# Optimization experiments

Measured on AMD Instinct MI355X. Metric: run time of the kernel, lower is better.

## Reference

```python
import jax, jax.numpy as jnp
import numpy as np

D = 128      # state_dim
ED = 20      # edge_dim (RBF basis size)
R = 3        # num message/update rounds
G = 3        # gated equivariant blocks
CUT = 5.0    # cutoff
N = 10000    # nodes
E = 160000   # edges
B = 500      # molecules
HRO = 64     # readout hidden


def setup_inputs() -> dict:
    key = jax.random.key(0)
    ks = jax.random.split(key, 40)
    sc = 0.05

    def nrm(k, shape):
        return jax.random.normal(k, shape, dtype=jnp.float32) * sc

    inp = {
        "h": jax.random.normal(ks[0], (N, 5), dtype=jnp.float32),
        "pos": jax.random.normal(ks[1], (N, 3), dtype=jnp.float32),
        "edge_index": jax.random.randint(ks[2], (2, E), 0, N),
        "batch": jnp.sort(jax.random.randint(ks[3], (N,), 0, B)),
        # node embedding Linear(5, D)
        "emb_w": nrm(ks[4], (5, D)), "emb_b": nrm(ks[5], (D,)),
        # per-round message params (stacked over rounds)
        "msg_phi_w1": nrm(ks[6], (R, D, D)), "msg_phi_b1": nrm(ks[7], (R, D)),
        "msg_phi_w2": nrm(ks[8], (R, D, 3 * D)), "msg_phi_b2": nrm(ks[9], (R, 3 * D)),
        "msg_filt_w": nrm(ks[10], (R, ED, 3 * D)), "msg_filt_b": nrm(ks[11], (R, 3 * D)),
        # per-round update params
        "upd_U": nrm(ks[12], (R, D, D)), "upd_V": nrm(ks[13], (R, D, D)),
        "upd_w1": nrm(ks[14], (R, 2 * D, D)), "upd_b1": nrm(ks[15], (R, D)),
        "upd_w2": nrm(ks[16], (R, D, 3 * D)), "upd_b2": nrm(ks[17], (R, 3 * D)),
        # gated equivariant blocks
        "geb_wv1": nrm(ks[18], (G, D, D)), "geb_wv2": nrm(ks[19], (G, D, D)),
        "geb_w1": nrm(ks[20], (G, 2 * D, D)), "geb_b1": nrm(ks[21], (G, D)),
        "geb_w2": nrm(ks[22], (G, D, 2 * D)), "geb_b2": nrm(ks[23], (G, 2 * D)),
        # invariant readout MLP
        "ro_w1": nrm(ks[24], (D, HRO)), "ro_b1": nrm(ks[25], (HRO,)),
        "ro_w2": nrm(ks[26], (HRO, 1)), "ro_b2": nrm(ks[27], (1,)),
    }
    return inp


def _safe_norm(x, axis):
    return jnp.sqrt(jnp.sum(x * x, axis=axis) + 1e-8)


def reference(h, pos, edge_index, batch,
              emb_w, emb_b,
              msg_phi_w1, msg_phi_b1, msg_phi_w2, msg_phi_b2,
              msg_filt_w, msg_filt_b,
              upd_U, upd_V, upd_w1, upd_b1, upd_w2, upd_b2,
              geb_wv1, geb_wv2, geb_w1, geb_b1, geb_w2, geb_b2,
              ro_w1, ro_b1, ro_w2, ro_b2):
    n_nodes = h.shape[0]
    row, col = edge_index[0], edge_index[1]
    # edge vectors: r_ij = pos[col] - pos[row]
    r_ij = pos[col] - pos[row]                                   # [E,3]
    d = jnp.clip(jnp.linalg.norm(r_ij, axis=1, keepdims=True), 1e-6, None)  # [E,1]
    unit = r_ij / d                                              # [E,3]
    # sinc radial basis + cosine cutoff
    freqs = jnp.arange(1, ED + 1, dtype=h.dtype)
    rbf = jnp.sin(freqs * jnp.pi * d / CUT) / d                  # [E,ED]
    fcut = 0.5 * (jnp.cos(jnp.pi * d / CUT) + 1.0) * (d < CUT)   # [E,1]

    s = h @ emb_w + emb_b                                        # [N,D]
    v = jnp.zeros((n_nodes, D, 3), dtype=h.dtype)                # [N,D,3]

    for r in range(R):
        # --- PaiNNMessage ---
        phi = jax.nn.silu(s @ msg_phi_w1[r] + msg_phi_b1[r]) @ msg_phi_w2[r] + msg_phi_b2[r]  # [N,3D]
        filt = (rbf @ msg_filt_w[r] + msg_filt_b[r]) * fcut      # [E,3D]
        x = phi[col] * filt                                      # gather + modulate  [E,3D]
        xs, xvv, xvw = jnp.split(x, 3, axis=-1)                  # each [E,D]
        ds = jax.ops.segment_sum(xs, row, num_segments=n_nodes)  # [N,D]
        dv_e = xvv[:, :, None] * v[col] + xvw[:, :, None] * unit[:, None, :]  # [E,D,3]
        dv = jax.ops.segment_sum(dv_e, row, num_segments=n_nodes)             # [N,D,3]
        s = s + ds
        v = v + dv
        # --- PaiNNUpdate ---
        Uv = jnp.einsum('ndc,de->nec', v, upd_U[r])              # [N,D,3]
        Vv = jnp.einsum('ndc,de->nec', v, upd_V[r])              # [N,D,3]
        Vn = _safe_norm(Vv, axis=-1)                             # [N,D]
        a = jax.nn.silu(jnp.concatenate([s, Vn], axis=-1) @ upd_w1[r] + upd_b1[r]) @ upd_w2[r] + upd_b2[r]
        a_ss, a_sv, a_vv = jnp.split(a, 3, axis=-1)
        s = s + a_ss + a_sv * jnp.sum(Uv * Vv, axis=-1)
        v = v + a_vv[:, :, None] * Uv

    # --- GatedEquivariantBlocks ---
    for g in range(G):
        v1 = jnp.einsum('ndc,de->nec', v, geb_wv1[g])
        v2 = jnp.einsum('ndc,de->nec', v, geb_wv2[g])
        n2 = _safe_norm(v2, axis=-1)                             # [N,D]
        a = jax.nn.silu(jnp.concatenate([s, n2], axis=-1) @ geb_w1[g] + geb_b1[g]) @ geb_w2[g] + geb_b2[g]
        s_new, gate = jnp.split(a, 2, axis=-1)
        s = s_new
        v = gate[:, :, None] * v1

    # --- InvariantReadout + molwise scatter ---
    out = jax.nn.silu(s @ ro_w1 + ro_b1) @ ro_w2 + ro_b2         # [N,1]
    molwise = jax.ops.segment_sum(out, batch, num_segments=B)    # [B,1]
    return molwise.squeeze(-1)
```

## Files before the change

### kernel.cpp

```cpp
#include <hip/hip_runtime.h>

typedef __attribute__((ext_vector_type(4))) float f32x4;
typedef __attribute__((ext_vector_type(8))) short short8;

#define D 128
#define D3 384
#define SLD 256
#define EDIM 20
#define KPAD 32
#define NR 3
#define NG 3
#define CUTOFF 5.0f
#define NNODES 10000
#define NEDGES 160000
#define NMOL 500
#define HROH 64
#define PI_F 3.14159265358979323846f

#define FBIAS 1
#define FSILU 2
#define FBF16O 4

static __device__ __forceinline__ float silu_f(float x) {
    return x / (1.0f + expf(-x));
}

static __device__ __forceinline__ ushort f2bf(float x) {
    uint u = __float_as_uint(x);
    uint r = (u + 0x7fffu + ((u >> 16) & 1u)) >> 16;
    return (ushort)r;
}
static __device__ __forceinline__ float bf2f(ushort h) {
    return __uint_as_float((uint)h << 16);
}
static __device__ __forceinline__ uint pack2(float a, float b) {
    return (uint)f2bf(a) | ((uint)f2bf(b) << 16);
}

#define TLR 64
#define TLC 64
#define KC 32
#define APAD 40
#define BPAD 36
#define CPAD 68

struct WSrc { const float* p[12]; };
#define WTOT 880640

__global__ __launch_bounds__(256) void wprep_k(WSrc ws, ushort* __restrict__ dh,
                                               ushort* __restrict__ dl)
{
    const int srcK[12] = {128,128, 20,128,128,256,128,128,128,256,128,128};
    const int dstK[12] = {128,128, 32,128,128,256,128,128,128,256,128,128};
    const int Mm[12]   = {128,384,384,128,128,128,384,128,128,128,256, 64};
    const int nm[12]   = {  3,  3,  3,  3,  3,  3,  3,  3,  3,  3,  3,  1};
    int i = blockIdx.x * 256 + threadIdx.x;
    if (i >= WTOT) return;
    int off = 0, seg = -1, loc = 0;
    #pragma unroll
    for (int s = 0; s < 12; ++s) {
        int sz = nm[s] * Mm[s] * dstK[s];
        if (seg < 0 && i < off + sz) { seg = s; loc = i - off; }
        off += sz;
    }
    int K = dstK[seg], M = Mm[seg], sK = srcK[seg];
    int mat = loc / (M * K);
    int rem = loc - mat * M * K;
    int m = rem / K, k = rem - m * K;
    float v = (k < sK) ? ws.p[seg][(size_t)(mat * sK + k) * M + m] : 0.f;
    ushort h = f2bf(v);
    dh[i] = h;
    dl[i] = f2bf(v - bf2f(h));
}

#define SEG_PHI_W1  0
#define SEG_PHI_W2  49152
#define SEG_FILT_W  196608
#define SEG_UPD_U   233472
#define SEG_UPD_V   282624
#define SEG_UPD_W1  331776
#define SEG_UPD_W2  430080
#define SEG_GEB_WV1 577536
#define SEG_GEB_WV2 626688
#define SEG_GEB_W1  675840
#define SEG_GEB_W2  774144
#define SEG_RO_W1   872448

__global__ __launch_bounds__(256) void gemm_k(
    const float* __restrict__ A, int lda,
    const ushort* __restrict__ Wh, const ushort* __restrict__ Wl, int ldk,
    const float* __restrict__ bias,
    float* __restrict__ C, ushort* __restrict__ Cbf, int ldc,
    int N, int K, int flags)
{
    const int n0 = blockIdx.x * TLR;
    const int m0 = blockIdx.y * TLC;
    __shared__ ushort SM[9728];
    ushort* Ah = SM;
    ushort* Al = SM + 2560;
    ushort* Bh = SM + 5120;
    ushort* Bl = SM + 7424;
    const int tid = threadIdx.x;
    const int arow = tid & 63;
    const int akq = (tid >> 6) * 4;
    const bool aok = (n0 + arow) < N;
    const float* Ar = A + (size_t)(n0 + arow) * lda;
    const int sm = tid & 63;
    const int sq = tid >> 6;
    const ushort* Wph = Wh + (size_t)(m0 + sm) * ldk + sq * 8;
    const ushort* Wpl = Wl + (size_t)(m0 + sm) * ldk + sq * 8;
    const int lane = tid & 63;
    const int wrow = (tid >> 6) * 16;
    const int fr = lane & 15;
    const int kg = lane >> 4;

    f32x4 acc[4];
    #pragma unroll
    for (int t = 0; t < 4; ++t) acc[t] = (f32x4){0.f, 0.f, 0.f, 0.f};

    for (int k0 = 0; k0 < K; k0 += KC) {
        #pragma unroll
        for (int half = 0; half < 2; ++half) {
            int kk = akq + half * 16;
            float4 v = aok ? *(const float4*)(Ar + k0 + kk)
                           : make_float4(0.f, 0.f, 0.f, 0.f);
            ushort h0 = f2bf(v.x), h1 = f2bf(v.y), h2 = f2bf(v.z), h3 = f2bf(v.w);
            ushort l0 = f2bf(v.x - bf2f(h0)), l1 = f2bf(v.y - bf2f(h1));
            ushort l2 = f2bf(v.z - bf2f(h2)), l3 = f2bf(v.w - bf2f(h3));
            uint2 ph, pl;
            ph.x = (uint)h0 | ((uint)h1 << 16); ph.y = (uint)h2 | ((uint)h3 << 16);
            pl.x = (uint)l0 | ((uint)l1 << 16); pl.y = (uint)l2 | ((uint)l3 << 16);
            *(uint2*)(Ah + arow * APAD + kk) = ph;
            *(uint2*)(Al + arow * APAD + kk) = pl;
        }
        {
            uint4 vh = *(const uint4*)(Wph + k0);
            uint4 vl = *(const uint4*)(Wpl + k0);
            ushort* dh = Bh + sm * BPAD + sq * 8;
            ushort* dl = Bl + sm * BPAD + sq * 8;
            *(uint2*)dh       = make_uint2(vh.x, vh.y);
            *(uint2*)(dh + 4) = make_uint2(vh.z, vh.w);
            *(uint2*)dl       = make_uint2(vl.x, vl.y);
            *(uint2*)(dl + 4) = make_uint2(vl.z, vl.w);
        }
        __syncthreads();
        short8 ah = *(const short8*)(Ah + (wrow + fr) * APAD + kg * 8);
        short8 al = *(const short8*)(Al + (wrow + fr) * APAD + kg * 8);
        #pragma unroll
        for (int t = 0; t < 4; ++t) {
            const ushort* bp = Bh + (t * 16 + fr) * BPAD + kg * 8;
            const ushort* bq = Bl + (t * 16 + fr) * BPAD + kg * 8;
            short8 bh, bl;
            ((uint2*)&bh)[0] = *(const uint2*)bp;
            ((uint2*)&bh)[1] = *(const uint2*)(bp + 4);
            ((uint2*)&bl)[0] = *(const uint2*)bq;
            ((uint2*)&bl)[1] = *(const uint2*)(bq + 4);
            acc[t] = __builtin_amdgcn_mfma_f32_16x16x32_bf16(ah, bh, acc[t], 0, 0, 0);
            acc[t] = __builtin_amdgcn_mfma_f32_16x16x32_bf16(al, bh, acc[t], 0, 0, 0);
            acc[t] = __builtin_amdgcn_mfma_f32_16x16x32_bf16(ah, bl, acc[t], 0, 0, 0);
        }
        __syncthreads();
    }

    if (flags & FBF16O) {
        float* Cs = (float*)SM;
        #pragma unroll
        for (int t = 0; t < 4; ++t) {
            #pragma unroll
            for (int r = 0; r < 4; ++r) {
                int row = wrow + kg * 4 + r;
                int n = n0 + row;
                int colm = t * 16 + fr;
                float val = 0.f;
                if (n < N) {
                    val = acc[t][r];
                    if (flags & FBIAS) val += bias[m0 + colm];
                    if (flags & FSILU) val = silu_f(val);
                }
                Cs[row * CPAD + colm] = val;
            }
        }
        __syncthreads();
        #pragma unroll
        for (int it = 0; it < 2; ++it) {
            int chunk = it * 256 + tid;
            int row = chunk >> 3;
            int c8 = (chunk & 7) * 8;
            int n = n0 + row;
            if (n < N) {
                const float* src = Cs + row * CPAD + c8;
                uint4 pk;
                pk.x = pack2(src[0], src[1]);
                pk.y = pack2(src[2], src[3]);
                pk.z = pack2(src[4], src[5]);
                pk.w = pack2(src[6], src[7]);
                *(uint4*)(Cbf + (size_t)n * ldc + m0 + c8) = pk;
            }
        }
    } else {
        #pragma unroll
        for (int t = 0; t < 4; ++t) {
            #pragma unroll
            for (int r = 0; r < 4; ++r) {
                int n = n0 + wrow + kg * 4 + r;
                if (n < N) {
                    int m = m0 + t * 16 + fr;
                    float val = acc[t][r];
                    if (flags & FBIAS) val += bias[m];
                    if (flags & FSILU) val = silu_f(val);
                    C[(size_t)n * ldc + m] = val;
                }
            }
        }
    }
}

__global__ __launch_bounds__(256) void filt_k(
    const float* __restrict__ RBFp,
    const ushort* __restrict__ Wfh,
    const float* __restrict__ bias,
    const float* __restrict__ uf_s,
    const int* __restrict__ col_s,
    const ushort* __restrict__ Pbf,
    ushort* __restrict__ X, int E)
{
    __shared__ ushort Ah[64 * APAD];
    __shared__ ushort Bs[D3 * BPAD];
    __shared__ float  Cs[64 * CPAD];
    __shared__ int    ColS[64];
    const int tid = threadIdx.x;
    const int e0 = blockIdx.x * 64;
    #pragma unroll
    for (int it = 0; it < 2; ++it) {
        int chunk = it * 256 + tid;
        int row = chunk >> 3;
        int kq = (chunk & 7) * 4;
        int e = e0 + row;
        float4 v = (e < E) ? *(const float4*)(RBFp + (size_t)e * KPAD + kq)
                           : make_float4(0.f, 0.f, 0.f, 0.f);
        uint2 ph;
        ph.x = pack2(v.x, v.y);
        ph.y = pack2(v.z, v.w);
        *(uint2*)(Ah + row * APAD + kq) = ph;
    }
    for (int m = tid; m < D3; m += 256) {
        const ushort* s = Wfh + (size_t)m * KPAD;
        ushort* dst = Bs + m * BPAD;
        #pragma unroll
        for (int q = 0; q < 2; ++q) {
            uint4 v = *(const uint4*)(s + q * 16);
            *(uint2*)(dst + q * 16)      = make_uint2(v.x, v.y);
            *(uint2*)(dst + q * 16 + 4)  = make_uint2(v.z, v.w);
            uint4 v2 = *(const uint4*)(s + q * 16 + 8);
            *(uint2*)(dst + q * 16 + 8)  = make_uint2(v2.x, v2.y);
            *(uint2*)(dst + q * 16 + 12) = make_uint2(v2.z, v2.w);
        }
    }
    if (tid < 64) {
        int e = e0 + tid;
        ColS[tid] = (e < E) ? col_s[e] : 0;
    }
    __syncthreads();

    const int lane = tid & 63;
    const int wrow = (tid >> 6) * 16;
    const int fr = lane & 15;
    const int kg = lane >> 4;
    short8 ah = *(const short8*)(Ah + (wrow + fr) * APAD + kg * 8);
    f32x4 acc[24];
    #pragma unroll
    for (int t = 0; t < 24; ++t) {
        const ushort* bp = Bs + (t * 16 + fr) * BPAD + kg * 8;
        short8 bh;
        ((uint2*)&bh)[0] = *(const uint2*)bp;
        ((uint2*)&bh)[1] = *(const uint2*)(bp + 4);
        acc[t] = __builtin_amdgcn_mfma_f32_16x16x32_bf16(
            ah, bh, (f32x4){0.f, 0.f, 0.f, 0.f}, 0, 0, 0);
    }
    float fc[4];
    #pragma unroll
    for (int r = 0; r < 4; ++r) {
        int e = e0 + wrow + kg * 4 + r;
        fc[r] = (e < E) ? uf_s[(size_t)e * 4 + 3] : 0.f;
    }
    for (int ct = 0; ct < 6; ++ct) {
        __syncthreads();
        #pragma unroll
        for (int tt = 0; tt < 4; ++tt) {
            int t = ct * 4 + tt;
            int colm = t * 16 + fr;
            float b = bias[colm];
            #pragma unroll
            for (int r = 0; r < 4; ++r) {
                int row = wrow + kg * 4 + r;
                Cs[row * CPAD + tt * 16 + fr] = (acc[t][r] + b) * fc[r];
            }
        }
        __syncthreads();
        #pragma unroll
        for (int it = 0; it < 2; ++it) {
            int chunk = it * 256 + tid;
            int row = chunk >> 3;
            int c8 = (chunk & 7) * 8;
            int e = e0 + row;
            if (e < E) {
                int mbase = ct * 64 + c8;
                int col = ColS[row];
                uint4 pg = *(const uint4*)(Pbf + (size_t)col * D3 + mbase);
                const float* src = Cs + row * CPAD + c8;
                uint4 pk;
                pk.x = pack2(src[0] * bf2f((ushort)(pg.x & 0xffff)),
                             src[1] * bf2f((ushort)(pg.x >> 16)));
                pk.y = pack2(src[2] * bf2f((ushort)(pg.y & 0xffff)),
                             src[3] * bf2f((ushort)(pg.y >> 16)));
                pk.z = pack2(src[4] * bf2f((ushort)(pg.z & 0xffff)),
                             src[5] * bf2f((ushort)(pg.z >> 16)));
                pk.w = pack2(src[6] * bf2f((ushort)(pg.w & 0xffff)),
                             src[7] * bf2f((ushort)(pg.w >> 16)));
                *(uint4*)(X + (size_t)e * D3 + mbase) = pk;
            }
        }
    }
}

template <bool WITHDOT>
__global__ __launch_bounds__(256) void uvn_k(
    const float* __restrict__ A,
    const ushort* __restrict__ WUh, const ushort* __restrict__ WUl,
    const ushort* __restrict__ WVh, const ushort* __restrict__ WVl,
    float* __restrict__ Uv,
    float* __restrict__ DOT,
    float* __restrict__ SX, int N)
{
    const int n0 = blockIdx.x * 32;
    const int m0 = blockIdx.y * 64;
    __shared__ ushort Ah[3][32 * APAD], Al[3][32 * APAD];
    __shared__ ushort Bh[2][64 * BPAD], Bl[2][64 * BPAD];
    const int tid = threadIdx.x;
    const int arow = tid & 31;
    const int akq = (tid >> 5) * 4;
    const bool aok = (n0 + arow) < N;
    const float* Ar = A + (size_t)(n0 + arow) * D3;
    const int sm = tid & 63;
    const int sq = tid >> 6;
    const int w = tid >> 6;
    const int rt = w & 1;
    const int ch = w >> 1;
    const int lane = tid & 63;
    const int fr = lane & 15;
    const int kg = lane >> 4;

    f32x4 acc[3][2][2];
    #pragma unroll
    for (int c = 0; c < 3; ++c)
        #pragma unroll
        for (int s = 0; s < 2; ++s)
            #pragma unroll
            for (int t = 0; t < 2; ++t) acc[c][s][t] = (f32x4){0.f, 0.f, 0.f, 0.f};

    for (int k0 = 0; k0 < D; k0 += KC) {
        #pragma unroll
        for (int c = 0; c < 3; ++c) {
            float4 v = aok ? *(const float4*)(Ar + c * D + k0 + akq)
                           : make_float4(0.f, 0.f, 0.f, 0.f);
            ushort h0 = f2bf(v.x), h1 = f2bf(v.y), h2 = f2bf(v.z), h3 = f2bf(v.w);
            ushort l0 = f2bf(v.x - bf2f(h0)), l1 = f2bf(v.y - bf2f(h1));
            ushort l2 = f2bf(v.z - bf2f(h2)), l3 = f2bf(v.w - bf2f(h3));
            uint2 ph, pl;
            ph.x = (uint)h0 | ((uint)h1 << 16); ph.y = (uint)h2 | ((uint)h3 << 16);
            pl.x = (uint)l0 | ((uint)l1 << 16); pl.y = (uint)l2 | ((uint)l3 << 16);
            *(uint2*)(&Ah[c][arow * APAD + akq]) = ph;
            *(uint2*)(&Al[c][arow * APAD + akq]) = pl;
        }
        #pragma unroll
        for (int s = 0; s < 2; ++s) {
            const ushort* sh = (s ? WVh : WUh) + (size_t)(m0 + sm) * D + k0 + sq * 8;
            const ushort* sl = (s ? WVl : WUl) + (size_t)(m0 + sm) * D + k0 + sq * 8;
            uint4 vh = *(const uint4*)sh;
            uint4 vl = *(const uint4*)sl;
            ushort* dh = &Bh[s][sm * BPAD + sq * 8];
            ushort* dl = &Bl[s][sm * BPAD + sq * 8];
            *(uint2*)dh       = make_uint2(vh.x, vh.y);
            *(uint2*)(dh + 4) = make_uint2(vh.z, vh.w);
            *(uint2*)dl       = make_uint2(vl.x, vl.y);
            *(uint2*)(dl + 4) = make_uint2(vl.z, vl.w);
        }
        __syncthreads();
        short8 ah[3], al[3];
        #pragma unroll
        for (int c = 0; c < 3; ++c) {
            ah[c] = *(const short8*)(&Ah[c][(rt * 16 + fr) * APAD + kg * 8]);
            al[c] = *(const short8*)(&Al[c][(rt * 16 + fr) * APAD + kg * 8]);
        }
        #pragma unroll
        for (int t = 0; t < 2; ++t) {
            #pragma unroll
            for (int s = 0; s < 2; ++s) {
                const ushort* bp = &Bh[s][(ch * 32 + t * 16 + fr) * BPAD + kg * 8];
                const ushort* bq = &Bl[s][(ch * 32 + t * 16 + fr) * BPAD + kg * 8];
                short8 bh, bl;
                ((uint2*)&bh)[0] = *(const uint2*)bp;
                ((uint2*)&bh)[1] = *(const uint2*)(bp + 4);
                ((uint2*)&bl)[0] = *(const uint2*)bq;
                ((uint2*)&bl)[1] = *(const uint2*)(bq + 4);
                #pragma unroll
                for (int c = 0; c < 3; ++c) {
                    acc[c][s][t] = __builtin_amdgcn_mfma_f32_16x16x32_bf16(ah[c], bh, acc[c][s][t], 0, 0, 0);
                    acc[c][s][t] = __builtin_amdgcn_mfma_f32_16x16x32_bf16(al[c], bh, acc[c][s][t], 0, 0, 0);
                    acc[c][s][t] = __builtin_amdgcn_mfma_f32_16x16x32_bf16(ah[c], bl, acc[c][s][t], 0, 0, 0);
                }
            }
        }
        __syncthreads();
    }
    #pragma unroll
    for (int t = 0; t < 2; ++t) {
        #pragma unroll
        for (int r = 0; r < 4; ++r) {
            int n = n0 + rt * 16 + kg * 4 + r;
            if (n < N) {
                int m = m0 + ch * 32 + t * 16 + fr;
                float ux = acc[0][0][t][r], uy = acc[1][0][t][r], uz = acc[2][0][t][r];
                float vx = acc[0][1][t][r], vy = acc[1][1][t][r], vz = acc[2][1][t][r];
                float* up = Uv + (size_t)n * D3 + m;
                up[0]     = ux;
                up[D]     = uy;
                up[2 * D] = uz;
                SX[(size_t)n * SLD + D + m] =
                    sqrtf(fmaf(vx, vx, fmaf(vy, vy, fmaf(vz, vz, 1e-8f))));
                if (WITHDOT)
                    DOT[(size_t)n * D + m] = fmaf(ux, vx, fmaf(uy, vy, uz * vz));
            }
        }
    }
}

__global__ __launch_bounds__(256) void emb_k(
    const float* __restrict__ h, const float* __restrict__ w,
    const float* __restrict__ b, float* __restrict__ s, int total)
{
    int i = blockIdx.x * 256 + threadIdx.x;
    if (i >= total) return;
    int n = i >> 7, d = i & 127;
    float acc = b[d];
    #pragma unroll
    for (int k = 0; k < 5; ++k) acc = fmaf(h[n * 5 + k], w[k * D + d], acc);
    s[(size_t)n * SLD + d] = acc;
}

__global__ __launch_bounds__(256) void hist_k(const int* __restrict__ ei,
                                              int* __restrict__ cnt, int E)
{
    int e = blockIdx.x * 256 + threadIdx.x;
    if (e < E) atomicAdd(&cnt[ei[e]], 1);
}

__global__ __launch_bounds__(256) void scan_k(const int* __restrict__ cnt,
                                              int* __restrict__ offs, int n)
{
    __shared__ int tmp[256];
    __shared__ int carry;
    if (threadIdx.x == 0) carry = 0;
    __syncthreads();
    for (int base = 0; base < n; base += 256) {
        int i = base + threadIdx.x;
        int v = (i < n) ? cnt[i] : 0;
        tmp[threadIdx.x] = v;
        __syncthreads();
        for (int off = 1; off < 256; off <<= 1) {
            int add = (threadIdx.x >= off) ? tmp[threadIdx.x - off] : 0;
            __syncthreads();
            tmp[threadIdx.x] += add;
            __syncthreads();
        }
        if (i < n) offs[i + 1] = carry + tmp[threadIdx.x];
        __syncthreads();
        if (threadIdx.x == 255) carry += tmp[255];
        __syncthreads();
    }
    if (threadIdx.x == 0) offs[0] = 0;
}

__global__ __launch_bounds__(256) void initnext_k(const int* __restrict__ offs,
                                                  int* __restrict__ next, int n)
{
    int i = blockIdx.x * 256 + threadIdx.x;
    if (i < n) next[i] = offs[i];
}

__global__ __launch_bounds__(256) void edge_pre_k(
    const int* __restrict__ ei, const float* __restrict__ pos,
    int* __restrict__ next, float* __restrict__ rbf_s,
    float* __restrict__ uf_s, int* __restrict__ col_s, int E)
{
    int e = blockIdx.x * 256 + threadIdx.x;
    if (e >= E) return;
    int r = ei[e], c = ei[E + e];
    float dx = pos[c * 3 + 0] - pos[r * 3 + 0];
    float dy = pos[c * 3 + 1] - pos[r * 3 + 1];
    float dz = pos[c * 3 + 2] - pos[r * 3 + 2];
    float dist = sqrtf(dx * dx + dy * dy + dz * dz);
    float d = fmaxf(dist, 1e-6f);
    float inv = 1.0f / d;
    int p = atomicAdd(&next[r], 1);
    col_s[p] = c;
    uf_s[p * 4 + 0] = dx * inv;
    uf_s[p * 4 + 1] = dy * inv;
    uf_s[p * 4 + 2] = dz * inv;
    uf_s[p * 4 + 3] = (d < CUTOFF) ? 0.5f * (cosf(PI_F * d / CUTOFF) + 1.0f) : 0.0f;
    float w = PI_F * d / CUTOFF;
    float* rb = rbf_s + (size_t)p * KPAD;
    #pragma unroll
    for (int k = 1; k <= EDIM; ++k)
        rb[k - 1] = sinf((float)k * w) * inv;
    #pragma unroll
    for (int k = EDIM; k < KPAD; ++k) rb[k] = 0.f;
}

#define MSG_NPB 2
__global__ __launch_bounds__(256) void message_csr_k(
    const int* __restrict__ offs, const int* __restrict__ col_s,
    const ushort* __restrict__ X, const float* __restrict__ uf_s,
    const float* __restrict__ Vold, const ushort* __restrict__ VbfOld,
    float* __restrict__ S, float* __restrict__ Vnew,
    ushort* __restrict__ VbfNew, int N)
{
    const int sub = threadIdx.x >> 7;
    const int d = threadIdx.x & 127;

    auto edge = [&](int j, float& ds, float& dvx, float& dvy, float& dvz) {
        const ushort* xp = X + (size_t)j * D3;
        float xs  = bf2f(xp[d]);
        float xvv = bf2f(xp[D + d]);
        float xvw = bf2f(xp[2 * D + d]);
        int col = col_s[j];
        float4 u4 = *(const float4*)(uf_s + (size_t)j * 4);
        const ushort* vc = VbfOld + (size_t)col * D3;
        ds += xs;
        dvx = fmaf(xvv, bf2f(vc[d]),         fmaf(xvw, u4.x, dvx));
        dvy = fmaf(xvv, bf2f(vc[D + d]),     fmaf(xvw, u4.y, dvy));
        dvz = fmaf(xvv, bf2f(vc[2 * D + d]), fmaf(xvw, u4.z, dvz));
    };

    int n = blockIdx.x * MSG_NPB + sub;
    if (n >= N) return;
    float ds0 = 0.f, dx0 = 0.f, dy0 = 0.f, dz0 = 0.f;
    float ds1 = 0.f, dx1 = 0.f, dy1 = 0.f, dz1 = 0.f;
    const int j0 = offs[n], j1 = offs[n + 1];
    int j = j0;
    for (; j + 2 <= j1; j += 2) {
        edge(j, ds0, dx0, dy0, dz0);
        edge(j + 1, ds1, dx1, dy1, dz1);
    }
    if (j < j1) edge(j, ds0, dx0, dy0, dz0);
    S[(size_t)n * SLD + d] += ds0 + ds1;
    const float* vo = Vold + (size_t)n * D3;
    float* vn = Vnew + (size_t)n * D3;
    ushort* vb = VbfNew + (size_t)n * D3;
    float nx = vo[d] + dx0 + dx1;
    float ny = vo[D + d] + dy0 + dy1;
    float nz = vo[2 * D + d] + dz0 + dz1;
    vn[d] = nx;         vb[d] = f2bf(nx);
    vn[D + d] = ny;     vb[D + d] = f2bf(ny);
    vn[2 * D + d] = nz; vb[2 * D + d] = f2bf(nz);
}

__global__ __launch_bounds__(256) void upd_apply_k(
    const float* __restrict__ U3, const float* __restrict__ DOT,
    const float* __restrict__ P, float* __restrict__ s,
    float* __restrict__ v, ushort* __restrict__ vbf, int total)
{
    int i = blockIdx.x * 256 + threadIdx.x;
    if (i >= total) return;
    int n = i >> 7, d = i & 127;
    const float* u = U3 + (size_t)n * D3;
    float ux = u[d], uy = u[D + d], uz = u[2 * D + d];
    const float* a = P + (size_t)n * D3;
    s[(size_t)n * SLD + d] += a[d] + a[D + d] * DOT[i];
    float avv = a[2 * D + d];
    float* vv = v + (size_t)n * D3;
    ushort* vb = vbf + (size_t)n * D3;
    float nx = fmaf(avv, ux, vv[d]);
    float ny = fmaf(avv, uy, vv[D + d]);
    float nz = fmaf(avv, uz, vv[2 * D + d]);
    vv[d] = nx;         vb[d] = f2bf(nx);
    vv[D + d] = ny;     vb[D + d] = f2bf(ny);
    vv[2 * D + d] = nz; vb[2 * D + d] = f2bf(nz);
}

__global__ __launch_bounds__(256) void geb_apply_k(
    const float* __restrict__ P, const float* __restrict__ U3,
    float* __restrict__ s, float* __restrict__ v, int total)
{
    int i = blockIdx.x * 256 + threadIdx.x;
    if (i >= total) return;
    int n = i >> 7, d = i & 127;
    const float* a = P + (size_t)n * 2 * D;
    s[(size_t)n * SLD + d] = a[d];
    float g = a[D + d];
    const float* u = U3 + (size_t)n * D3;
    float* vv = v + (size_t)n * D3;
    vv[d]         = g * u[d];
    vv[D + d]     = g * u[D + d];
    vv[2 * D + d] = g * u[2 * D + d];
}

__global__ __launch_bounds__(256) void readout_k(
    const float* __restrict__ H2, const float* __restrict__ w2,
    const float* __restrict__ b2, const int* __restrict__ batch,
    float* __restrict__ out, int N)
{
    int n = blockIdx.x * 256 + threadIdx.x;
    if (n >= N) return;
    float acc = b2[0];
    const float* hrow = H2 + (size_t)n * HROH;
    #pragma unroll
    for (int k = 0; k < HROH; ++k) acc = fmaf(hrow[k], w2[k], acc);
    atomicAdd(out + batch[n], acc);
}


static inline void gemm(hipStream_t st, const float* A, int lda,
                        const ushort* Wh, const ushort* Wl, int ldk,
                        const float* bias,
                        float* C, ushort* Cbf, int ldc,
                        int N, int K, int M, int flags)
{
    dim3 g((N + TLR - 1) / TLR, M / TLC, 1);
    hipLaunchKernelGGL(gemm_k, g, dim3(256), 0, st,
                       A, lda, Wh, Wl, ldk, bias, C, Cbf, ldc, N, K, flags);
}

extern "C" void kernel_launch(void* const* d_in, const int* in_sizes, int n_in,
                              void* d_out, int out_size, void* d_ws, size_t ws_size,
                              hipStream_t stream)
{
    const float* h          = (const float*)d_in[0];
    const float* pos        = (const float*)d_in[1];
    const int*   ei         = (const int*)d_in[2];
    const int*   batch      = (const int*)d_in[3];
    const float* emb_w      = (const float*)d_in[4];
    const float* emb_b      = (const float*)d_in[5];
    const float* msg_phi_w1 = (const float*)d_in[6];
    const float* msg_phi_b1 = (const float*)d_in[7];
    const float* msg_phi_w2 = (const float*)d_in[8];
    const float* msg_phi_b2 = (const float*)d_in[9];
    const float* msg_filt_w = (const float*)d_in[10];
    const float* msg_filt_b = (const float*)d_in[11];
    const float* upd_U      = (const float*)d_in[12];
    const float* upd_V      = (const float*)d_in[13];
    const float* upd_w1     = (const float*)d_in[14];
    const float* upd_b1     = (const float*)d_in[15];
    const float* upd_w2     = (const float*)d_in[16];
    const float* upd_b2     = (const float*)d_in[17];
    const float* geb_wv1    = (const float*)d_in[18];
    const float* geb_wv2    = (const float*)d_in[19];
    const float* geb_w1     = (const float*)d_in[20];
    const float* geb_b1     = (const float*)d_in[21];
    const float* geb_w2     = (const float*)d_in[22];
    const float* geb_b2     = (const float*)d_in[23];
    const float* ro_w1      = (const float*)d_in[24];
    const float* ro_b1      = (const float*)d_in[25];
    const float* ro_w2      = (const float*)d_in[26];
    const float* ro_b2      = (const float*)d_in[27];
    float* out = (float*)d_out;

    const int N = NNODES, E = NEDGES;

    char* p = (char*)d_ws;
    auto carve = [&](size_t bytes) {
        char* r = p;
        p += (bytes + 255) & ~(size_t)255;
        return r;
    };
    float*  SX   = (float*)carve((size_t)N * SLD * 4);
    float*  VA   = (float*)carve((size_t)N * D3 * 4);
    float*  VB   = (float*)carve((size_t)N * D3 * 4);
    float*  P_   = (float*)carve((size_t)N * D3 * 4);
    ushort* Pbf  = (ushort*)P_;
    ushort* VBFa = (ushort*)carve((size_t)N * D3 * 2);
    ushort* VBFb = (ushort*)carve((size_t)N * D3 * 2);
    float*  H    = (float*)carve((size_t)N * D * 4);
    float*  H2   = (float*)carve((size_t)N * D * 4);
    float*  RBFp = (float*)carve((size_t)E * KPAD * 4);
    float*  UFs  = (float*)carve((size_t)E * 4 * 4);
    int*    COLs = (int*)carve((size_t)E * 4);
    int*    offs = (int*)carve((size_t)(N + 1) * 4);
    int*    nxt  = (int*)carve((size_t)N * 4);
    ushort* WTH  = (ushort*)carve((size_t)WTOT * 2);
    ushort* WTL  = (ushort*)carve((size_t)WTOT * 2);
    ushort* X    = (ushort*)carve((size_t)E * D3 * 2);

    WSrc wsrc;
    wsrc.p[0] = msg_phi_w1; wsrc.p[1] = msg_phi_w2; wsrc.p[2] = msg_filt_w;
    wsrc.p[3] = upd_U;      wsrc.p[4] = upd_V;      wsrc.p[5] = upd_w1;
    wsrc.p[6] = upd_w2;     wsrc.p[7] = geb_wv1;    wsrc.p[8] = geb_wv2;
    wsrc.p[9] = geb_w1;     wsrc.p[10] = geb_w2;    wsrc.p[11] = ro_w1;
    hipLaunchKernelGGL(wprep_k, dim3((WTOT + 255) / 256), dim3(256), 0, stream,
                       wsrc, WTH, WTL);

    hipMemsetAsync(VA, 0, (size_t)N * D3 * 4, stream);
    hipMemsetAsync(VBFa, 0, (size_t)N * D3 * 2, stream);
    hipLaunchKernelGGL(emb_k, dim3((N * D + 255) / 256), dim3(256), 0, stream,
                       h, emb_w, emb_b, SX, N * D);
    hipMemsetAsync(nxt, 0, (size_t)N * 4, stream);
    hipLaunchKernelGGL(hist_k, dim3((E + 255) / 256), dim3(256), 0, stream, ei, nxt, E);
    hipLaunchKernelGGL(scan_k, dim3(1), dim3(256), 0, stream, nxt, offs, N);
    hipLaunchKernelGGL(initnext_k, dim3((N + 255) / 256), dim3(256), 0, stream,
                       offs, nxt, N);
    hipLaunchKernelGGL(edge_pre_k, dim3((E + 255) / 256), dim3(256), 0, stream,
                       ei, pos, nxt, RBFp, UFs, COLs, E);

    float*  Vc = VA;   ushort* VbfC = VBFa;
    float*  Vs = VB;   ushort* VbfS = VBFb;

    for (int r = 0; r < NR; ++r) {
        gemm(stream, SX, SLD, WTH + SEG_PHI_W1 + (size_t)r * D * D,
             WTL + SEG_PHI_W1 + (size_t)r * D * D, D,
             msg_phi_b1 + (size_t)r * D, H, nullptr, D, N, D, D, FBIAS | FSILU);
        gemm(stream, H, D, WTH + SEG_PHI_W2 + (size_t)r * D * D3,
             WTL + SEG_PHI_W2 + (size_t)r * D * D3, D,
             msg_phi_b2 + (size_t)r * D3, nullptr, Pbf, D3, N, D, D3,
             FBIAS | FBF16O);
        hipLaunchKernelGGL(filt_k, dim3((E + 63) / 64), dim3(256), 0, stream,
                           RBFp, WTH + SEG_FILT_W + (size_t)r * KPAD * D3,
                           msg_filt_b + (size_t)r * D3, UFs, COLs, Pbf, X, E);
        hipLaunchKernelGGL(message_csr_k, dim3((N + MSG_NPB - 1) / MSG_NPB),
                           dim3(256), 0, stream,
                           offs, COLs, X, UFs, Vc, VbfC, SX, Vs, VbfS, N);
        { float* t = Vc; Vc = Vs; Vs = t; }
        { ushort* t = VbfC; VbfC = VbfS; VbfS = t; }
        float* Uv = Vs;
        hipLaunchKernelGGL(HIP_KERNEL_NAME(uvn_k<true>),
                           dim3((N + 31) / 32, 2), dim3(256), 0, stream,
                           Vc, WTH + SEG_UPD_U + (size_t)r * D * D,
                           WTL + SEG_UPD_U + (size_t)r * D * D,
                           WTH + SEG_UPD_V + (size_t)r * D * D,
                           WTL + SEG_UPD_V + (size_t)r * D * D,
                           Uv, H, SX, N);
        gemm(stream, SX, SLD, WTH + SEG_UPD_W1 + (size_t)r * 2 * D * D,
             WTL + SEG_UPD_W1 + (size_t)r * 2 * D * D, 2 * D,
             upd_b1 + (size_t)r * D, H2, nullptr, D, N, 2 * D, D, FBIAS | FSILU);
        gemm(stream, H2, D, WTH + SEG_UPD_W2 + (size_t)r * D * D3,
             WTL + SEG_UPD_W2 + (size_t)r * D * D3, D,
             upd_b2 + (size_t)r * D3, P_, nullptr, D3, N, D, D3, FBIAS);
        hipLaunchKernelGGL(upd_apply_k, dim3((N * D + 255) / 256), dim3(256), 0,
                           stream, Uv, H, P_, SX, Vc, VbfC, N * D);
    }

    for (int g = 0; g < NG; ++g) {
        float* Uv = Vs;
        hipLaunchKernelGGL(HIP_KERNEL_NAME(uvn_k<false>),
                           dim3((N + 31) / 32, 2), dim3(256), 0, stream,
                           Vc, WTH + SEG_GEB_WV1 + (size_t)g * D * D,
                           WTL + SEG_GEB_WV1 + (size_t)g * D * D,
                           WTH + SEG_GEB_WV2 + (size_t)g * D * D,
                           WTL + SEG_GEB_WV2 + (size_t)g * D * D,
                           Uv, nullptr, SX, N);
        gemm(stream, SX, SLD, WTH + SEG_GEB_W1 + (size_t)g * 2 * D * D,
             WTL + SEG_GEB_W1 + (size_t)g * 2 * D * D, 2 * D,
             geb_b1 + (size_t)g * D, H2, nullptr, D, N, 2 * D, D, FBIAS | FSILU);
        gemm(stream, H2, D, WTH + SEG_GEB_W2 + (size_t)g * D * 2 * D,
             WTL + SEG_GEB_W2 + (size_t)g * D * 2 * D, D,
             geb_b2 + (size_t)g * 2 * D, P_, nullptr, 2 * D, N, D, 2 * D, FBIAS);
        hipLaunchKernelGGL(geb_apply_k, dim3((N * D + 255) / 256), dim3(256), 0,
                           stream, P_, Uv, SX, Vc, N * D);
    }

    gemm(stream, SX, SLD, WTH + SEG_RO_W1, WTL + SEG_RO_W1, D,
         ro_b1, H2, nullptr, HROH, N, D, HROH, FBIAS | FSILU);
    hipMemsetAsync(out, 0, (size_t)NMOL * 4, stream);
    hipLaunchKernelGGL(readout_k, dim3((N + 255) / 256), dim3(256), 0, stream,
                       H2, ro_w2, ro_b2, batch, out, N);
}
```

Before: 872.9 us.

## Fuse two-layer MLP GEMM pairs into a single kernel with hidden kept in LDS

Adds a templated mlp_k kernel that computes Linear+SiLU then Linear for a 32-row tile, storing the hidden activation as split bf16 hi/lo in shared memory instead of writing it to global memory. It replaces the phi, update and gated-block GEMM pairs, removing one launch and the H/H2 round-trip per MLP. The cost is fewer blocks (N/32 with one block per row tile), the first-layer weights being reloaded by every block, and a serial loop over output column groups, which may reduce parallelism compared with the 2D-gridded GEMMs.

```diff
diff --git a/kernel.cpp b/kernel.cpp
--- a/kernel.cpp
+++ b/kernel.cpp
@@ -85,6 +85,203 @@
 #define SEG_GEB_W1  675840
 #define SEG_GEB_W2  774144
 #define SEG_RO_W1   872448
+
+template <int K1, int M2, bool OUTBF>
+__global__ __launch_bounds__(256) void mlp_k(
+    const float* __restrict__ A, int lda,
+    const ushort* __restrict__ W1h, const ushort* __restrict__ W1l,
+    const float* __restrict__ b1,
+    const ushort* __restrict__ W2h, const ushort* __restrict__ W2l,
+    const float* __restrict__ b2,
+    float* __restrict__ C, ushort* __restrict__ Cbf, int N)
+{
+    __shared__ char SMB[27648 + 17408];
+    ushort* Ah  = (ushort*)SMB;
+    ushort* Al  = Ah + 1280;
+    ushort* B1h = Ah + 2560;
+    ushort* B1l = B1h + 4608;
+    ushort* Hh  = (ushort*)(SMB + 27648);
+    ushort* Hl  = Hh + 4352;
+
+    const int tid = threadIdx.x;
+    const int n0 = blockIdx.x * 32;
+    const int w = tid >> 6;
+    const int rt = w & 1;
+    const int ch = w >> 1;
+    const int lane = tid & 63;
+    const int fr = lane & 15;
+    const int kg = lane >> 4;
+    const int arow = tid & 31;
+    const int akq = (tid >> 5) * 4;
+    const bool aok = (n0 + arow) < N;
+    const float* Ar = A + (size_t)(n0 + arow) * lda;
+    const int bcol = tid & 127;
+    const int bhalf = tid >> 7;
+
+    f32x4 acc1[4];
+    #pragma unroll
+    for (int t = 0; t < 4; ++t) acc1[t] = (f32x4){0.f, 0.f, 0.f, 0.f};
+
+    for (int k0 = 0; k0 < K1; k0 += KC) {
+        {
+            float4 v = aok ? *(const float4*)(Ar + k0 + akq)
+                           : make_float4(0.f, 0.f, 0.f, 0.f);
+            ushort h0 = f2bf(v.x), h1 = f2bf(v.y), h2 = f2bf(v.z), h3 = f2bf(v.w);
+            ushort l0 = f2bf(v.x - bf2f(h0)), l1 = f2bf(v.y - bf2f(h1));
+            ushort l2 = f2bf(v.z - bf2f(h2)), l3 = f2bf(v.w - bf2f(h3));
+            uint2 ph, pl;
+            ph.x = (uint)h0 | ((uint)h1 << 16); ph.y = (uint)h2 | ((uint)h3 << 16);
+            pl.x = (uint)l0 | ((uint)l1 << 16); pl.y = (uint)l2 | ((uint)l3 << 16);
+            *(uint2*)(Ah + arow * APAD + akq) = ph;
+            *(uint2*)(Al + arow * APAD + akq) = pl;
+        }
+        {
+            const ushort* sh = W1h + (size_t)bcol * K1 + k0 + bhalf * 16;
+            const ushort* sl = W1l + (size_t)bcol * K1 + k0 + bhalf * 16;
+            ushort* dh = B1h + bcol * BPAD + bhalf * 16;
+            ushort* dl = B1l + bcol * BPAD + bhalf * 16;
+            uint4 v0 = *(const uint4*)sh;
+            uint4 v1 = *(const uint4*)(sh + 8);
+            *(uint2*)dh       = make_uint2(v0.x, v0.y);
+            *(uint2*)(dh + 4) = make_uint2(v0.z, v0.w);
+            *(uint2*)(dh + 8) = make_uint2(v1.x, v1.y);
+            *(uint2*)(dh + 12)= make_uint2(v1.z, v1.w);
+            uint4 u0 = *(const uint4*)sl;
+            uint4 u1 = *(const uint4*)(sl + 8);
+            *(uint2*)dl       = make_uint2(u0.x, u0.y);
+            *(uint2*)(dl + 4) = make_uint2(u0.z, u0.w);
+            *(uint2*)(dl + 8) = make_uint2(u1.x, u1.y);
+            *(uint2*)(dl + 12)= make_uint2(u1.z, u1.w);
+        }
+        __syncthreads();
+        short8 ah = *(const short8*)(Ah + (rt * 16 + fr) * APAD + kg * 8);
+        short8 al = *(const short8*)(Al + (rt * 16 + fr) * APAD + kg * 8);
+        #pragma unroll
+        for (int t = 0; t < 4; ++t) {
+            const ushort* bp = B1h + (ch * 64 + t * 16 + fr) * BPAD + kg * 8;
+            const ushort* bq = B1l + (ch * 64 + t * 16 + fr) * BPAD + kg * 8;
+            short8 bh, bl;
+            ((uint2*)&bh)[0] = *(const uint2*)bp;
+            ((uint2*)&bh)[1] = *(const uint2*)(bp + 4);
+            ((uint2*)&bl)[0] = *(const uint2*)bq;
+            ((uint2*)&bl)[1] = *(const uint2*)(bq + 4);
+            acc1[t] = __builtin_amdgcn_mfma_f32_16x16x32_bf16(ah, bh, acc1[t], 0, 0, 0);
+            acc1[t] = __builtin_amdgcn_mfma_f32_16x16x32_bf16(al, bh, acc1[t], 0, 0, 0);
+            acc1[t] = __builtin_amdgcn_mfma_f32_16x16x32_bf16(ah, bl, acc1[t], 0, 0, 0);
+        }
+        __syncthreads();
+    }
+    #pragma unroll
+    for (int t = 0; t < 4; ++t) {
+        int colm = ch * 64 + t * 16 + fr;
+        float b = b1[colm];
+        #pragma unroll
+        for (int r = 0; r < 4; ++r) {
+            int row = rt * 16 + kg * 4 + r;
+            float hv = silu_f(acc1[t][r] + b);
+            ushort hh = f2bf(hv);
+            Hh[row * 136 + colm] = hh;
+            Hl[row * 136 + colm] = f2bf(hv - bf2f(hh));
+        }
+    }
+    __syncthreads();
+
+    ushort* B2h = (ushort*)SMB;
+    ushort* B2l = B2h + 4608;
+    const int NG2 = M2 / 128;
+    for (int g = 0; g < NG2; ++g) {
+        f32x4 acc2[4];
+        #pragma unroll
+        for (int t = 0; t < 4; ++t) acc2[t] = (f32x4){0.f, 0.f, 0.f, 0.f};
+        for (int k0 = 0; k0 < D; k0 += KC) {
+            {
+                const ushort* sh = W2h + (size_t)(g * 128 + bcol) * D + k0 + bhalf * 16;
+                const ushort* sl = W2l + (size_t)(g * 128 + bcol) * D + k0 + bhalf * 16;
+                ushort* dh = B2h + bcol * BPAD + bhalf * 16;
+                ushort* dl = B2l + bcol * BPAD + bhalf * 16;
+                uint4 v0 = *(const uint4*)sh;
+                uint4 v1 = *(const uint4*)(sh + 8);
+                *(uint2*)dh       = make_uint2(v0.x, v0.y);
+                *(uint2*)(dh + 4) = make_uint2(v0.z, v0.w);
+                *(uint2*)(dh + 8) = make_uint2(v1.x, v1.y);
+                *(uint2*)(dh + 12)= make_uint2(v1.z, v1.w);
+                uint4 u0 = *(const uint4*)sl;
+                uint4 u1 = *(const uint4*)(sl + 8);
+                *(uint2*)dl       = make_uint2(u0.x, u0.y);
+                *(uint2*)(dl + 4) = make_uint2(u0.z, u0.w);
+                *(uint2*)(dl + 8) = make_uint2(u1.x, u1.y);
+                *(uint2*)(dl + 12)= make_uint2(u1.z, u1.w);
+            }
+            __syncthreads();
+            short8 ah, al;
+            {
+                const ushort* hp = Hh + (rt * 16 + fr) * 136 + k0 + kg * 8;
+                const ushort* hq = Hl + (rt * 16 + fr) * 136 + k0 + kg * 8;
+                ((uint2*)&ah)[0] = *(const uint2*)hp;
+                ((uint2*)&ah)[1] = *(const uint2*)(hp + 4);
+                ((uint2*)&al)[0] = *(const uint2*)hq;
+                ((uint2*)&al)[1] = *(const uint2*)(hq + 4);
+            }
+            #pragma unroll
+            for (int t = 0; t < 4; ++t) {
+                const ushort* bp = B2h + (ch * 64 + t * 16 + fr) * BPAD + kg * 8;
+                const ushort* bq = B2l + (ch * 64 + t * 16 + fr) * BPAD + kg * 8;
+                short8 bh, bl;
+                ((uint2*)&bh)[0] = *(const uint2*)bp;
+                ((uint2*)&bh)[1] = *(const uint2*)(bp + 4);
+                ((uint2*)&bl)[0] = *(const uint2*)bq;
+                ((uint2*)&bl)[1] = *(const uint2*)(bq + 4);
+                acc2[t] = __builtin_amdgcn_mfma_f32_16x16x32_bf16(ah, bh, acc2[t], 0, 0, 0);
+                acc2[t] = __builtin_amdgcn_mfma_f32_16x16x32_bf16(al, bh, acc2[t], 0, 0, 0);
+                acc2[t] = __builtin_amdgcn_mfma_f32_16x16x32_bf16(ah, bl, acc2[t], 0, 0, 0);
+            }
+            __syncthreads();
+        }
+        if (OUTBF) {
+            float* Cs = (float*)SMB;
+            #pragma unroll
+            for (int t = 0; t < 4; ++t) {
+                int colm = ch * 64 + t * 16 + fr;
+                float b = b2[g * 128 + colm];
+                #pragma unroll
+                for (int r = 0; r < 4; ++r) {
+                    int row = rt * 16 + kg * 4 + r;
+                    Cs[row * CPAD + colm] = acc2[t][r] + b;
+                }
+            }
+            __syncthreads();
+            #pragma unroll
+            for (int it = 0; it < 2; ++it) {
+                int chunk = it * 256 + tid;
+                int row = chunk >> 4;
+                int c8 = (chunk & 15) * 8;
+                int n = n0 + row;
+                if (n < N) {
+                    const float* src = Cs + row * CPAD + c8;
+                    uint4 pk;
+                    pk.x = pack2(src[0], src[1]);
+                    pk.y = pack2(src[2], src[3]);
+                    pk.z = pack2(src[4], src[5]);
+                    pk.w = pack2(src[6], src[7]);
+                    *(uint4*)(Cbf + (size_t)n * M2 + g * 128 + c8) = pk;
+                }
+            }
+            __syncthreads();
+        } else {
+            #pragma unroll
+            for (int t = 0; t < 4; ++t) {
+                int colm = ch * 64 + t * 16 + fr;
+                float b = b2[g * 128 + colm];
+                #pragma unroll
+                for (int r = 0; r < 4; ++r) {
+                    int n = n0 + rt * 16 + kg * 4 + r;
+                    if (n < N)
+                        C[(size_t)n * M2 + g * 128 + colm] = acc2[t][r] + b;
+                }
+            }
+        }
+    }
+}
 
 __global__ __launch_bounds__(256) void gemm_k(
     const float* __restrict__ A, int lda,
@@ -162,54 +359,17 @@
         __syncthreads();
     }
 
-    if (flags & FBF16O) {
-        float* Cs = (float*)SM;
-        #pragma unroll
-        for (int t = 0; t < 4; ++t) {
-            #pragma unroll
-            for (int r = 0; r < 4; ++r) {
-                int row = wrow + kg * 4 + r;
-                int n = n0 + row;
-                int colm = t * 16 + fr;
-                float val = 0.f;
-                if (n < N) {
-                    val = acc[t][r];
-                    if (flags & FBIAS) val += bias[m0 + colm];
-                    if (flags & FSILU) val = silu_f(val);
-                }
-                Cs[row * CPAD + colm] = val;
-            }
-        }
-        __syncthreads();
-        #pragma unroll
-        for (int it = 0; it < 2; ++it) {
-            int chunk = it * 256 + tid;
-            int row = chunk >> 3;
-            int c8 = (chunk & 7) * 8;
-            int n = n0 + row;
+    #pragma unroll
+    for (int t = 0; t < 4; ++t) {
+        #pragma unroll
+        for (int r = 0; r < 4; ++r) {
+            int n = n0 + wrow + kg * 4 + r;
             if (n < N) {
-                const float* src = Cs + row * CPAD + c8;
-                uint4 pk;
-                pk.x = pack2(src[0], src[1]);
-                pk.y = pack2(src[2], src[3]);
-                pk.z = pack2(src[4], src[5]);
-                pk.w = pack2(src[6], src[7]);
-                *(uint4*)(Cbf + (size_t)n * ldc + m0 + c8) = pk;
-            }
-        }
-    } else {
-        #pragma unroll
-        for (int t = 0; t < 4; ++t) {
-            #pragma unroll
-            for (int r = 0; r < 4; ++r) {
-                int n = n0 + wrow + kg * 4 + r;
-                if (n < N) {
-                    int m = m0 + t * 16 + fr;
-                    float val = acc[t][r];
-                    if (flags & FBIAS) val += bias[m];
-                    if (flags & FSILU) val = silu_f(val);
-                    C[(size_t)n * ldc + m] = val;
-                }
+                int m = m0 + t * 16 + fr;
+                float val = acc[t][r];
+                if (flags & FBIAS) val += bias[m];
+                if (flags & FSILU) val = silu_f(val);
+                C[(size_t)n * ldc + m] = val;
             }
         }
     }
@@ -619,17 +779,6 @@
     atomicAdd(out + batch[n], acc);
 }
 
-
-static inline void gemm(hipStream_t st, const float* A, int lda,
-                        const ushort* Wh, const ushort* Wl, int ldk,
-                        const float* bias,
-                        float* C, ushort* Cbf, int ldc,
-                        int N, int K, int M, int flags)
-{
-    dim3 g((N + TLR - 1) / TLR, M / TLC, 1);
-    hipLaunchKernelGGL(gemm_k, g, dim3(256), 0, st,
-                       A, lda, Wh, Wl, ldk, bias, C, Cbf, ldc, N, K, flags);
-}
 
 extern "C" void kernel_launch(void* const* d_in, const int* in_sizes, int n_in,
                               void* d_out, int out_size, void* d_ws, size_t ws_size,
@@ -713,15 +862,19 @@
 
     float*  Vc = VA;   ushort* VbfC = VBFa;
     float*  Vs = VB;   ushort* VbfS = VBFb;
+    const int MB = (N + 31) / 32;
 
     for (int r = 0; r < NR; ++r) {
-        gemm(stream, SX, SLD, WTH + SEG_PHI_W1 + (size_t)r * D * D,
-             WTL + SEG_PHI_W1 + (size_t)r * D * D, D,
-             msg_phi_b1 + (size_t)r * D, H, nullptr, D, N, D, D, FBIAS | FSILU);
-        gemm(stream, H, D, WTH + SEG_PHI_W2 + (size_t)r * D * D3,
-             WTL + SEG_PHI_W2 + (size_t)r * D * D3, D,
-             msg_phi_b2 + (size_t)r * D3, nullptr, Pbf, D3, N, D, D3,
-             FBIAS | FBF16O);
+        hipLaunchKernelGGL(HIP_KERNEL_NAME(mlp_k<128, 384, true>),
+                           dim3(MB), dim3(256), 0, stream,
+                           SX, SLD,
+                           WTH + SEG_PHI_W1 + (size_t)r * D * D,
+                           WTL + SEG_PHI_W1 + (size_t)r * D * D,
+                           msg_phi_b1 + (size_t)r * D,
+                           WTH + SEG_PHI_W2 + (size_t)r * D * D3,
+                           WTL + SEG_PHI_W2 + (size_t)r * D * D3,
+                           msg_phi_b2 + (size_t)r * D3,
+                           nullptr, Pbf, N);
         hipLaunchKernelGGL(filt_k, dim3((E + 63) / 64), dim3(256), 0, stream,
                            RBFp, WTH + SEG_FILT_W + (size_t)r * KPAD * D3,
                            msg_filt_b + (size_t)r * D3, UFs, COLs, Pbf, X, E);
@@ -732,18 +885,22 @@
         { ushort* t = VbfC; VbfC = VbfS; VbfS = t; }
         float* Uv = Vs;
         hipLaunchKernelGGL(HIP_KERNEL_NAME(uvn_k<true>),
-                           dim3((N + 31) / 32, 2), dim3(256), 0, stream,
+                           dim3(MB, 2), dim3(256), 0, stream,
                            Vc, WTH + SEG_UPD_U + (size_t)r * D * D,
                            WTL + SEG_UPD_U + (size_t)r * D * D,
                            WTH + SEG_UPD_V + (size_t)r * D * D,
                            WTL + SEG_UPD_V + (size_t)r * D * D,
                            Uv, H, SX, N);
-        gemm(stream, SX, SLD, WTH + SEG_UPD_W1 + (size_t)r * 2 * D * D,
-             WTL + SEG_UPD_W1 + (size_t)r * 2 * D * D, 2 * D,
-             upd_b1 + (size_t)r * D, H2, nullptr, D, N, 2 * D, D, FBIAS | FSILU);
-        gemm(stream, H2, D, WTH + SEG_UPD_W2 + (size_t)r * D * D3,
-             WTL + SEG_UPD_W2 + (size_t)r * D * D3, D,
-             upd_b2 + (size_t)r * D3, P_, nullptr, D3, N, D, D3, FBIAS);
+        hipLaunchKernelGGL(HIP_KERNEL_NAME(mlp_k<256, 384, false>),
+                           dim3(MB), dim3(256), 0, stream,
+                           SX, SLD,
+                           WTH + SEG_UPD_W1 + (size_t)r * 2 * D * D,
+                           WTL + SEG_UPD_W1 + (size_t)r * 2 * D * D,
+                           upd_b1 + (size_t)r * D,
+                           WTH + SEG_UPD_W2 + (size_t)r * D * D3,
+                           WTL + SEG_UPD_W2 + (size_t)r * D * D3,
+                           upd_b2 + (size_t)r * D3,
+                           P_, nullptr, N);
         hipLaunchKernelGGL(upd_apply_k, dim3((N * D + 255) / 256), dim3(256), 0,
                            stream, Uv, H, P_, SX, Vc, VbfC, N * D);
     }
@@ -751,24 +908,32 @@
     for (int g = 0; g < NG; ++g) {
         float* Uv = Vs;
         hipLaunchKernelGGL(HIP_KERNEL_NAME(uvn_k<false>),
-                           dim3((N + 31) / 32, 2), dim3(256), 0, stream,
+                           dim3(MB, 2), dim3(256), 0, stream,
                            Vc, WTH + SEG_GEB_WV1 + (size_t)g * D * D,
                            WTL + SEG_GEB_WV1 + (size_t)g * D * D,
                            WTH + SEG_GEB_WV2 + (size_t)g * D * D,
                            WTL + SEG_GEB_WV2 + (size_t)g * D * D,
                            Uv, nullptr, SX, N);
-        gemm(stream, SX, SLD, WTH + SEG_GEB_W1 + (size_t)g * 2 * D * D,
-             WTL + SEG_GEB_W1 + (size_t)g * 2 * D * D, 2 * D,
-             geb_b1 + (size_t)g * D, H2, nullptr, D, N, 2 * D, D, FBIAS | FSILU);
-        gemm(stream, H2, D, WTH + SEG_GEB_W2 + (size_t)g * D * 2 * D,
-             WTL + SEG_GEB_W2 + (size_t)g * D * 2 * D, D,
-             geb_b2 + (size_t)g * 2 * D, P_, nullptr, 2 * D, N, D, 2 * D, FBIAS);
+        hipLaunchKernelGGL(HIP_KERNEL_NAME(mlp_k<256, 256, false>),
+                           dim3(MB), dim3(256), 0, stream,
+                           SX, SLD,
+                           WTH + SEG_GEB_W1 + (size_t)g * 2 * D * D,
+                           WTL + SEG_GEB_W1 + (size_t)g * 2 * D * D,
+                           geb_b1 + (size_t)g * D,
+                           WTH + SEG_GEB_W2 + (size_t)g * D * 2 * D,
+                           WTL + SEG_GEB_W2 + (size_t)g * D * 2 * D,
+                           geb_b2 + (size_t)g * 2 * D,
+                           P_, nullptr, N);
         hipLaunchKernelGGL(geb_apply_k, dim3((N * D + 255) / 256), dim3(256), 0,
                            stream, P_, Uv, SX, Vc, N * D);
     }
 
-    gemm(stream, SX, SLD, WTH + SEG_RO_W1, WTL + SEG_RO_W1, D,
-         ro_b1, H2, nullptr, HROH, N, D, HROH, FBIAS | FSILU);
+    {
+        dim3 grd((N + TLR - 1) / TLR, HROH / TLC > 0 ? HROH / TLC : 1, 1);
+        hipLaunchKernelGGL(gemm_k, grd, dim3(256), 0, stream,
+                           SX, SLD, WTH + SEG_RO_W1, WTL + SEG_RO_W1, D,
+                           ro_b1, H2, nullptr, HROH, N, D, FBIAS | FSILU);
+    }
     hipMemsetAsync(out, 0, (size_t)NMOL * 4, stream);
     hipLaunchKernelGGL(readout_k, dim3((N + 255) / 256), dim3(256), 0, stream,
                        H2, ro_w2, ro_b2, batch, out, N);
```

Result: faster. 849.2 us (-2.7%).
